# Optimization experiments

Hardware: AMD Instinct MI355X
Metric: run time of the kernel (lower is better)

## Reference

```python
import jax, jax.numpy as jnp
from jax import lax
import numpy as np

B, T, D_IN, H, D_L1_IN = 128, 2048, 5, 128, 256


def _gru_layer(x, w_ih, w_hh, b_ih, b_hh, reverse):
    # x: [B,T,D]; w_ih: [3H,D]; w_hh: [3H,H]. PyTorch gate order: r, z, n.
    gx = jnp.einsum('btd,gd->btg', x, w_ih) + b_ih  # [B,T,3H] input projections, batched
    if reverse:
        gx = gx[:, ::-1]
    gx_t = jnp.swapaxes(gx, 0, 1)  # [T,B,3H]
    h0 = jnp.zeros((x.shape[0], H), x.dtype)

    def step(h, gxt):
        gh = h @ w_hh.T + b_hh  # [B,3H]
        r = jax.nn.sigmoid(gxt[:, :H] + gh[:, :H])
        z = jax.nn.sigmoid(gxt[:, H:2 * H] + gh[:, H:2 * H])
        n = jnp.tanh(gxt[:, 2 * H:] + r * gh[:, 2 * H:])
        h_new = (1.0 - z) * n + z * h
        return h_new, h_new

    _, ys = lax.scan(step, h0, gx_t)  # ys: [T,B,H]
    ys = jnp.swapaxes(ys, 0, 1)  # [B,T,H]
    if reverse:
        ys = ys[:, ::-1]
    return ys


def setup_inputs() -> dict:
    key = jax.random.key(0)
    ks = jax.random.split(key, 16)
    s0 = 1.0 / np.sqrt(H)

    def w(k, shape):
        return jax.random.uniform(k, shape, jnp.float32, -s0, s0)

    inp = {'seq': jax.random.normal(ks[0], (B, T, D_IN), jnp.float32)}
    # layer 0 forward / backward (input dim 5)
    inp['w_ih_l0f'] = w(ks[1], (3 * H, D_IN)); inp['w_hh_l0f'] = w(ks[2], (3 * H, H))
    inp['b_ih_l0f'] = w(ks[3], (3 * H,));      inp['b_hh_l0f'] = w(ks[4], (3 * H,))
    inp['w_ih_l0b'] = w(ks[5], (3 * H, D_IN)); inp['w_hh_l0b'] = w(ks[6], (3 * H, H))
    inp['b_ih_l0b'] = w(ks[7], (3 * H,));      inp['b_hh_l0b'] = w(ks[8], (3 * H,))
    # layer 1 forward / backward (input dim 256 = 2*H)
    inp['w_ih_l1f'] = w(ks[9], (3 * H, D_L1_IN));  inp['w_hh_l1f'] = w(ks[10], (3 * H, H))
    inp['b_ih_l1f'] = w(ks[11], (3 * H,));         inp['b_hh_l1f'] = w(ks[12], (3 * H,))
    inp['w_ih_l1b'] = w(ks[13], (3 * H, D_L1_IN)); inp['w_hh_l1b'] = w(ks[14], (3 * H, H))
    inp['b_ih_l1b'] = w(ks[15], (3 * H,));         inp['b_hh_l1b'] = w(ks[15], (3 * H,)) * 0.9
    # linear head
    kf = jax.random.split(ks[0], 2)
    inp['fc_w'] = w(kf[0], (1, 2 * H))
    inp['fc_b'] = w(kf[1], (1,))
    return inp


def reference(seq, w_ih_l0f, w_hh_l0f, b_ih_l0f, b_hh_l0f,
              w_ih_l0b, w_hh_l0b, b_ih_l0b, b_hh_l0b,
              w_ih_l1f, w_hh_l1f, b_ih_l1f, b_hh_l1f,
              w_ih_l1b, w_hh_l1b, b_ih_l1b, b_hh_l1b,
              fc_w, fc_b):
    # layer 0: bidirectional, concat directions
    y0f = _gru_layer(seq, w_ih_l0f, w_hh_l0f, b_ih_l0f, b_hh_l0f, reverse=False)
    y0b = _gru_layer(seq, w_ih_l0b, w_hh_l0b, b_ih_l0b, b_hh_l0b, reverse=True)
    y0 = jnp.concatenate([y0f, y0b], axis=-1)  # [B,T,256]
    # layer 1
    y1f = _gru_layer(y0, w_ih_l1f, w_hh_l1f, b_ih_l1f, b_hh_l1f, reverse=False)
    y1b = _gru_layer(y0, w_ih_l1b, w_hh_l1b, b_ih_l1b, b_hh_l1b, reverse=True)
    y1 = jnp.concatenate([y1f, y1b], axis=-1)  # [B,T,256]
    # head on last timestep
    return y1[:, -1, :] @ fc_w.T + fc_b  # [B,1]
```

## Files before the change

### kernel.cpp

```cpp
#include <hip/hip_runtime.h>
#include <hip/hip_fp16.h>
#include <cstdint>

#define B_   128
#define T_   2048
#define DIN  5
#define H_   128
#define G3   384
#define D1   256
#define CH   128
#define NCH  (T_ / CH)
#define LOG2CH 7
#define NTILE (B_ * CH / 128 * 6)
#define NGB   248

typedef _Float16 half8 __attribute__((ext_vector_type(8)));
typedef float f32x4 __attribute__((ext_vector_type(4)));

__device__ __forceinline__ float sigmoid_f(float x) {
    return __builtin_amdgcn_rcpf(1.0f + __expf(-x));
}
__device__ __forceinline__ float tanh_f(float x) {
    return 1.0f - 2.0f * __builtin_amdgcn_rcpf(__expf(2.0f * x) + 1.0f);
}
__device__ __forceinline__ unsigned long long pack4h(const float* h) {
    union { __half2 h2[2]; unsigned long long u; } pk;
    pk.h2[0] = __floats2half2_rn(h[0], h[1]);
    pk.h2[1] = __floats2half2_rn(h[2], h[3]);
    return pk.u;
}
__device__ __forceinline__ f32x4 h4_to_f(unsigned long long u) {
    union { unsigned long long u; __half2 h2[2]; } p; p.u = u;
    const float2 a = __half22float2(p.h2[0]);
    const float2 b = __half22float2(p.h2[1]);
    f32x4 r; r[0] = a.x; r[1] = a.y; r[2] = b.x; r[3] = b.y; return r;
}
__device__ __forceinline__ void fast_barrier() {
    asm volatile("s_waitcnt lgkmcnt(0)\n\ts_barrier" ::: "memory");
}

__global__ __launch_bounds__(512, 2) void scan0_mfma4(
    const float* __restrict__ seq,
    const float* __restrict__ wihf, const float* __restrict__ whhf,
    const float* __restrict__ bihf, const float* __restrict__ bhhf,
    const float* __restrict__ wihb, const float* __restrict__ whhb,
    const float* __restrict__ bihb, const float* __restrict__ bhhb,
    __half* __restrict__ y0)
{
    const int tid = threadIdx.x;
    const int w  = tid >> 6;
    const int l  = tid & 63;
    const int lo = l & 15;
    const int g  = l >> 4;
    const int dir = blockIdx.x >> 3;
    const int bg  = blockIdx.x & 7;

    const float* w_ih = dir ? wihb : wihf;
    const float* w_hh = dir ? whhb : whhf;
    const float* b_ih = dir ? bihb : bihf;
    const float* b_hh = dir ? bhhb : bhhf;

    __shared__ __align__(16) char smem[2 * 16 * 512];

    half8 a_r[5], a_z[5], a_n[5], a_x;
    {
        const int grow = w * 16 + lo;
#pragma unroll
        for (int c = 0; c < 5; ++c) {
            half8 vr, vz, vn;
#pragma unroll
            for (int j = 0; j < 8; ++j) {
                const int k = c * 32 + g * 8 + j;
                float fr, fz, fn;
                if (k < 128) {
                    fr = w_hh[grow * H_ + k];
                    fz = w_hh[(128 + grow) * H_ + k];
                    fn = w_hh[(256 + grow) * H_ + k];
                } else if (k < 133) {
                    fr = w_ih[grow * DIN + (k - 128)];
                    fz = w_ih[(128 + grow) * DIN + (k - 128)];
                    fn = 0.f;
                } else if (k == 133) {
                    fr = b_ih[grow] + b_hh[grow];
                    fz = b_ih[128 + grow] + b_hh[128 + grow];
                    fn = b_hh[256 + grow];
                } else { fr = 0.f; fz = 0.f; fn = 0.f; }
                vr[j] = (_Float16)fr; vz[j] = (_Float16)fz; vn[j] = (_Float16)fn;
            }
            a_r[c] = vr; a_z[c] = vz; a_n[c] = vn;
        }
        half8 vx;
#pragma unroll
        for (int j = 0; j < 8; ++j) {
            const int k = 128 + g * 8 + j;
            float f = 0.f;
            if (k < 133)       f = w_ih[(256 + grow) * DIN + (k - 128)];
            else if (k == 133) f = b_ih[256 + grow];
            vx[j] = (_Float16)f;
        }
        a_x = vx;
    }

#pragma unroll
    for (int q = 0; q < 2; ++q) {
        f32x4 z = {0.f, 0.f, 0.f, 0.f};
        *reinterpret_cast<f32x4*>(smem + tid * 32 + q * 16) = z;
    }
    __syncthreads();
    if (tid < 32) {
        const int row = tid & 15, bu = tid >> 4;
        *(_Float16*)(smem + bu * 8192 + row * 512 + (266 ^ ((row & 7) << 4))) =
            (_Float16)1.0f;
    }
    const bool stager = tid < 80;
    const int sb = tid / 5, sd = tid % 5;
    const size_t seqbase = (size_t)(bg * 16 + sb) * T_ * DIN + sd;
    float x_t1 = 0.f;
    if (stager) {
        const int tt0 = dir ? (T_ - 1) : 0;
        const float x0 = seq[seqbase + (size_t)tt0 * DIN];
        *(_Float16*)(smem + sb * 512 + ((256 + 2 * sd) ^ ((sb & 7) << 4))) =
            (_Float16)x0;
        const int tt1 = dir ? (T_ - 2) : 1;
        x_t1 = seq[seqbase + (size_t)tt1 * DIN];
    }
    __syncthreads();

    float h_old[4];
#pragma unroll
    for (int q = 0; q < 4; ++q) h_old[q] = 0.f;

    for (int t = 0; t < T_; ++t) {
        char* cur = smem + (t & 1) * 8192;
        char* nxt = smem + ((t + 1) & 1) * 8192;

        if (stager)
            *(_Float16*)(nxt + sb * 512 + ((256 + 2 * sd) ^ ((sb & 7) << 4))) =
                (_Float16)x_t1;

        half8 bf[5];
#pragma unroll
        for (int c = 0; c < 5; ++c)
            bf[c] = *reinterpret_cast<const half8*>(
                cur + lo * 512 + ((c * 64 + g * 16) ^ ((lo & 7) << 4)));

        float x_t2 = 0.f;
        if (stager) {
            const int t2 = (t + 2 < T_) ? t + 2 : T_ - 1;
            const int tt2 = dir ? (T_ - 1 - t2) : t2;
            x_t2 = seq[seqbase + (size_t)tt2 * DIN];
        }

        f32x4 zr = {0.f, 0.f, 0.f, 0.f};
        f32x4 accr = zr, accz = zr, accn = zr, accx;
#pragma unroll
        for (int c = 0; c < 5; ++c) {
            accr = __builtin_amdgcn_mfma_f32_16x16x32_f16(a_r[c], bf[c], accr, 0, 0, 0);
            accz = __builtin_amdgcn_mfma_f32_16x16x32_f16(a_z[c], bf[c], accz, 0, 0, 0);
            accn = __builtin_amdgcn_mfma_f32_16x16x32_f16(a_n[c], bf[c], accn, 0, 0, 0);
        }
        accx = __builtin_amdgcn_mfma_f32_16x16x32_f16(a_x, bf[4], zr, 0, 0, 0);

        const int tt = dir ? (T_ - 1 - t) : t;
        {
            float hn[4];
#pragma unroll
            for (int q = 0; q < 4; ++q) {
                const float r = sigmoid_f(accr[q]);
                const float z = sigmoid_f(accz[q]);
                const float n = tanh_f(accx[q] + r * accn[q]);
                hn[q] = n + z * (h_old[q] - n);
                h_old[q] = hn[q];
            }
            const int j0 = w * 16 + g * 4;
            const unsigned long long pu = pack4h(hn);
            *reinterpret_cast<unsigned long long*>(
                &y0[((size_t)(bg * 16 + lo) * T_ + tt) * D1 + dir * H_ + j0]) = pu;
            *reinterpret_cast<unsigned long long*>(
                nxt + lo * 512 + ((2 * j0) ^ ((lo & 7) << 4))) = pu;
        }
        x_t1 = x_t2;
        fast_barrier();
    }
}

__device__ __forceinline__ void scan1_role(
    char* smem,
    const __half* __restrict__ gxc,
    const float* __restrict__ whh, const float* __restrict__ bhh,
    float* __restrict__ h1, int c)
{
    __builtin_amdgcn_s_setprio(1);

    const int tid = threadIdx.x;
    const int w = tid >> 6, l = tid & 63;
    const int lo = l & 15, g = l >> 4;
    const int grp = blockIdx.x;

    half8 a_r[2][4], a_z[2][4], a_n[2][4];
    float br[2][4], bz[2][4], bn[2][4];
#pragma unroll
    for (int i = 0; i < 2; ++i) {
        const int grow = (2 * w + i) * 16 + lo;
#pragma unroll
        for (int cc = 0; cc < 4; ++cc) {
            half8 vr, vz, vn;
#pragma unroll
            for (int j = 0; j < 8; ++j) {
                const int k = cc * 32 + g * 8 + j;
                vr[j] = (_Float16)whh[grow * H_ + k];
                vz[j] = (_Float16)whh[(128 + grow) * H_ + k];
                vn[j] = (_Float16)whh[(256 + grow) * H_ + k];
            }
            a_r[i][cc] = vr; a_z[i][cc] = vz; a_n[i][cc] = vn;
        }
#pragma unroll
        for (int q = 0; q < 4; ++q) {
            const int gq = (2 * w + i) * 16 + g * 4 + q;
            br[i][q] = bhh[gq];
            bz[i][q] = bhh[128 + gq];
            bn[i][q] = bhh[256 + gq];
        }
    }

#pragma unroll
    for (int q = 0; q < 2; ++q) {
        f32x4 z = {0.f, 0.f, 0.f, 0.f};
        *reinterpret_cast<f32x4*>(smem + tid * 32 + q * 16) = z;
    }
    __syncthreads();

    float h_old[2][4];
    if (c == 0) {
#pragma unroll
        for (int i = 0; i < 2; ++i)
#pragma unroll
            for (int q = 0; q < 4; ++q) h_old[i][q] = 0.f;
    } else {
#pragma unroll
        for (int i = 0; i < 2; ++i) {
            const int j0 = (2 * w + i) * 16 + g * 4;
            const f32x4 hv = *reinterpret_cast<const f32x4*>(
                &h1[(grp * 16 + lo) * H_ + j0]);
            float hn[4];
#pragma unroll
            for (int q = 0; q < 4; ++q) { h_old[i][q] = hv[q]; hn[q] = hv[q]; }
            *reinterpret_cast<unsigned long long*>(
                smem + lo * 256 + ((2 * j0) ^ ((lo & 7) << 4))) = pack4h(hn);
        }
    }
    __syncthreads();

    const __half* gxl = gxc + (size_t)(grp * 16 + lo) * CH * G3;
    unsigned long long gxc_cur[6], gxc_nxt[6];
#pragma unroll
    for (int i = 0; i < 2; ++i) {
        const int gr0 = (2 * w + i) * 16 + g * 4;
        gxc_cur[i]     = *reinterpret_cast<const unsigned long long*>(gxl + gr0);
        gxc_cur[2 + i] = *reinterpret_cast<const unsigned long long*>(gxl + 128 + gr0);
        gxc_cur[4 + i] = *reinterpret_cast<const unsigned long long*>(gxl + 256 + gr0);
    }

    for (int t = 0; t < CH; ++t) {
        char* curb = smem + (t & 1) * 4096;
        char* nxtb = smem + ((t + 1) & 1) * 4096;

        half8 bf[4];
#pragma unroll
        for (int cc = 0; cc < 4; ++cc)
            bf[cc] = *reinterpret_cast<const half8*>(
                curb + lo * 256 + ((cc * 64 + g * 16) ^ ((lo & 7) << 4)));

        const int tn = (t + 1 < CH) ? t + 1 : t;
        const __half* p = gxl + (size_t)tn * G3;
#pragma unroll
        for (int i = 0; i < 2; ++i) {
            const int gr0 = (2 * w + i) * 16 + g * 4;
            gxc_nxt[i]     = *reinterpret_cast<const unsigned long long*>(p + gr0);
            gxc_nxt[2 + i] = *reinterpret_cast<const unsigned long long*>(p + 128 + gr0);
            gxc_nxt[4 + i] = *reinterpret_cast<const unsigned long long*>(p + 256 + gr0);
        }

        f32x4 accr[2], accz[2], accn[2];
#pragma unroll
        for (int i = 0; i < 2; ++i) {
            f32x4 zr = {0.f, 0.f, 0.f, 0.f};
            accr[i] = zr; accz[i] = zr; accn[i] = zr;
#pragma unroll
            for (int cc = 0; cc < 4; ++cc) {
                accr[i] = __builtin_amdgcn_mfma_f32_16x16x32_f16(a_r[i][cc], bf[cc], accr[i], 0, 0, 0);
                accz[i] = __builtin_amdgcn_mfma_f32_16x16x32_f16(a_z[i][cc], bf[cc], accz[i], 0, 0, 0);
                accn[i] = __builtin_amdgcn_mfma_f32_16x16x32_f16(a_n[i][cc], bf[cc], accn[i], 0, 0, 0);
            }
        }

#pragma unroll
        for (int i = 0; i < 2; ++i) {
            const f32x4 gr = h4_to_f(gxc_cur[i]);
            const f32x4 gz = h4_to_f(gxc_cur[2 + i]);
            const f32x4 gn = h4_to_f(gxc_cur[4 + i]);
            float hn[4];
#pragma unroll
            for (int q = 0; q < 4; ++q) {
                const float r = sigmoid_f(accr[i][q] + br[i][q] + gr[q]);
                const float z = sigmoid_f(accz[i][q] + bz[i][q] + gz[q]);
                const float n = tanh_f(gn[q] + r * (accn[i][q] + bn[i][q]));
                hn[q] = n + z * (h_old[i][q] - n);
                h_old[i][q] = hn[q];
            }
            const int j0 = (2 * w + i) * 16 + g * 4;
            *reinterpret_cast<unsigned long long*>(
                nxtb + lo * 256 + ((2 * j0) ^ ((lo & 7) << 4))) = pack4h(hn);
        }
#pragma unroll
        for (int i = 0; i < 6; ++i) gxc_cur[i] = gxc_nxt[i];
        fast_barrier();
    }

#pragma unroll
    for (int i = 0; i < 2; ++i) {
        const int j0 = (2 * w + i) * 16 + g * 4;
        f32x4 hv;
#pragma unroll
        for (int q = 0; q < 4; ++q) hv[q] = h_old[i][q];
        *reinterpret_cast<f32x4*>(&h1[(grp * 16 + lo) * H_ + j0]) = hv;
    }
    __builtin_amdgcn_s_setprio(0);
}

__device__ __forceinline__ void gemm_role(
    char* smem, int rb,
    const __half* __restrict__ A, const float* __restrict__ W,
    const float* __restrict__ bias, __half* __restrict__ C, int c0)
{
    _Float16 (*As)[32] = reinterpret_cast<_Float16(*)[32]>(smem);
    _Float16 (*Bs)[32] = reinterpret_cast<_Float16(*)[32]>(smem + 8192);
    const int tid = threadIdx.x;
    const int wave = tid >> 6, l = tid & 63;
    const int wm = wave >> 1, wn = wave & 1;
    const int lo = l & 15, g = l >> 4;
    const int m0 = (rb & 127) * 128, n0 = (rb >> 7) * 64;

    f32x4 acc[4][2];
#pragma unroll
    for (int mt = 0; mt < 4; ++mt)
#pragma unroll
        for (int nt = 0; nt < 2; ++nt) {
            f32x4 z = {0.f, 0.f, 0.f, 0.f};
            acc[mt][nt] = z;
        }

    for (int kc = 0; kc < 256; kc += 32) {
#pragma unroll
        for (int r2 = 0; r2 < 2; ++r2) {
            const int idx = tid + r2 * 256;
            const int row = idx >> 2, seg = idx & 3;
            const int m = m0 + row, bb = m >> LOG2CH, tlq = m & (CH - 1);
            const __half* src = A + ((size_t)bb * T_ + c0 + tlq) * D1 + kc + seg * 8;
            *reinterpret_cast<uint4*>(&As[row][seg * 8]) =
                *reinterpret_cast<const uint4*>(src);
        }
        {
            const int row = tid >> 2, seg = tid & 3;
            const float* srcw = W + (size_t)(n0 + row) * D1 + kc + seg * 8;
            const float4 u0 = *reinterpret_cast<const float4*>(srcw);
            const float4 u1 = *reinterpret_cast<const float4*>(srcw + 4);
            half8 hv;
            hv[0] = (_Float16)u0.x; hv[1] = (_Float16)u0.y;
            hv[2] = (_Float16)u0.z; hv[3] = (_Float16)u0.w;
            hv[4] = (_Float16)u1.x; hv[5] = (_Float16)u1.y;
            hv[6] = (_Float16)u1.z; hv[7] = (_Float16)u1.w;
            *reinterpret_cast<half8*>(&Bs[row][seg * 8]) = hv;
        }
        __syncthreads();
        half8 af[4], bfr[2];
#pragma unroll
        for (int mt = 0; mt < 4; ++mt)
            af[mt] = *reinterpret_cast<half8*>(&As[wm * 64 + mt * 16 + lo][g * 8]);
#pragma unroll
        for (int nt = 0; nt < 2; ++nt)
            bfr[nt] = *reinterpret_cast<half8*>(&Bs[wn * 32 + nt * 16 + lo][g * 8]);
#pragma unroll
        for (int mt = 0; mt < 4; ++mt)
#pragma unroll
            for (int nt = 0; nt < 2; ++nt)
                acc[mt][nt] = __builtin_amdgcn_mfma_f32_16x16x32_f16(
                    af[mt], bfr[nt], acc[mt][nt], 0, 0, 0);
        __syncthreads();
    }
#pragma unroll
    for (int nt = 0; nt < 2; ++nt) {
        const int n = n0 + wn * 32 + nt * 16 + lo;
        const float bv = bias[n];
#pragma unroll
        for (int mt = 0; mt < 4; ++mt) {
            const int mrow = m0 + wm * 64 + mt * 16 + g * 4;
#pragma unroll
            for (int q = 0; q < 4; ++q)
                C[(size_t)(mrow + q) * G3 + n] = __float2half(acc[mt][nt][q] + bv);
        }
    }
}

__global__ __launch_bounds__(256, 1) void fused_l1(
    const __half* __restrict__ y0,
    const float* __restrict__ W1f, const float* __restrict__ b1f,
    __half* __restrict__ gbufA, __half* __restrict__ gbufB,
    const float* __restrict__ whh, const float* __restrict__ bhh,
    float* __restrict__ h1, int ci_scan, int ci_gemm)
{
    __shared__ __align__(16) char smem[12288];
    if (blockIdx.x < 8) {
        if (ci_scan >= 0) {
            const __half* gxc = (ci_scan & 1) ? gbufB : gbufA;
            scan1_role(smem, gxc, whh, bhh, h1, ci_scan);
        }
    } else {
        if (ci_gemm < NCH) {
            __half* gxc = (ci_gemm & 1) ? gbufB : gbufA;
            for (int rb = (int)blockIdx.x - 8; rb < NTILE; rb += NGB)
                gemm_role(smem, rb, y0, W1f, b1f, gxc, ci_gemm * CH);
        }
    }
}

__global__ __launch_bounds__(384, 1) void back1_fc(
    const __half* __restrict__ y0, const float* __restrict__ h1,
    const float* __restrict__ w_ih_1b, const float* __restrict__ b_ih_1b,
    const float* __restrict__ b_hh_1b,
    const float* __restrict__ fc_w, const float* __restrict__ fc_b,
    float* __restrict__ out)
{
    const int g = threadIdx.x;
    const int b = blockIdx.x;
    __shared__ float ylast[D1];
    __shared__ float pre_rz[2 * H_];
    __shared__ float gxn[H_], ghn[H_];
    __shared__ float hb[H_];
    __shared__ float red[H_];

    if (g < D1) ylast[g] = __half2float(y0[((size_t)b * T_ + (T_ - 1)) * D1 + g]);
    __syncthreads();

    float accb = b_ih_1b[g];
    const float* wrow = w_ih_1b + (size_t)g * D1;
#pragma unroll 8
    for (int k = 0; k < D1; k += 4) {
        const float4 v = *reinterpret_cast<const float4*>(&ylast[k]);
        const float4 wv = *reinterpret_cast<const float4*>(&wrow[k]);
        accb += v.x * wv.x + v.y * wv.y + v.z * wv.z + v.w * wv.w;
    }
    const float bh2 = b_hh_1b[g];
    if (g < 2 * H_) pre_rz[g] = accb + bh2;
    else            { gxn[g - 2 * H_] = accb; ghn[g - 2 * H_] = bh2; }
    __syncthreads();
    if (g < H_) {
        const float r = sigmoid_f(pre_rz[g]);
        const float z = sigmoid_f(pre_rz[g + H_]);
        const float n = tanh_f(gxn[g] + r * ghn[g]);
        hb[g] = (1.0f - z) * n;
    }
    __syncthreads();
    if (g < H_) red[g] = h1[b * H_ + g] * fc_w[g] + hb[g] * fc_w[H_ + g];
    __syncthreads();
    if (g == 0) {
        float s = fc_b[0];
#pragma unroll 8
        for (int k = 0; k < H_; ++k) s += red[k];
        out[b] = s;
    }
}

extern "C" void kernel_launch(void* const* d_in, const int* in_sizes, int n_in,
                              void* d_out, int out_size, void* d_ws, size_t ws_size,
                              hipStream_t stream)
{
    const float* seq      = (const float*)d_in[0];
    const float* w_ih_l0f = (const float*)d_in[1];
    const float* w_hh_l0f = (const float*)d_in[2];
    const float* b_ih_l0f = (const float*)d_in[3];
    const float* b_hh_l0f = (const float*)d_in[4];
    const float* w_ih_l0b = (const float*)d_in[5];
    const float* w_hh_l0b = (const float*)d_in[6];
    const float* b_ih_l0b = (const float*)d_in[7];
    const float* b_hh_l0b = (const float*)d_in[8];
    const float* w_ih_l1f = (const float*)d_in[9];
    const float* w_hh_l1f = (const float*)d_in[10];
    const float* b_ih_l1f = (const float*)d_in[11];
    const float* b_hh_l1f = (const float*)d_in[12];
    const float* w_ih_l1b = (const float*)d_in[13];
    const float* b_ih_l1b = (const float*)d_in[15];
    const float* b_hh_l1b = (const float*)d_in[16];
    const float* fc_w     = (const float*)d_in[17];
    const float* fc_b     = (const float*)d_in[18];
    float* out = (float*)d_out;

    const size_t y0_bytes = (size_t)B_ * T_ * D1 * sizeof(__half);
    const size_t gx_bytes = (size_t)B_ * CH * G3 * sizeof(__half);
    __half* y0h   = (__half*)d_ws;
    __half* gbufA = (__half*)((char*)d_ws + y0_bytes);
    __half* gbufB = (__half*)((char*)d_ws + y0_bytes + gx_bytes);
    float*  h1    = (float*)((char*)d_ws + y0_bytes + 2 * gx_bytes);

    hipLaunchKernelGGL(scan0_mfma4, dim3(16), dim3(512), 0, stream,
        seq, w_ih_l0f, w_hh_l0f, b_ih_l0f, b_hh_l0f,
             w_ih_l0b, w_hh_l0b, b_ih_l0b, b_hh_l0b, y0h);

    for (int i = 0; i <= NCH; ++i) {
        hipLaunchKernelGGL(fused_l1, dim3(8 + NGB), dim3(256), 0, stream,
            y0h, w_ih_l1f, b_ih_l1f, gbufA, gbufB,
            w_hh_l1f, b_hh_l1f, h1, i - 1, i);
    }

    hipLaunchKernelGGL(back1_fc, dim3(B_), dim3(384), 0, stream,
        y0h, h1, w_ih_l1b, b_ih_l1b, b_hh_l1b, fc_w, fc_b, out);
}
```

Measured before the change: 3.443 ms.

## Replace per-chunk layer-1 launches with one persistent kernel using flag sync

The 17 per-chunk launches of the fused layer-1 kernel become a single persistent kernel. Scan blocks and GEMM blocks now coordinate through global atomic counters: scan blocks spin until a chunk's GEMM is done, and GEMM blocks wait until the scan has consumed the buffer from two chunks earlier. The scan keeps its hidden state in registers across chunks instead of round-tripping through global memory. This removes kernel-launch and tail overhead and lets the GEMM run ahead, but it relies on all 256 blocks being co-resident and adds spin-wait and fence costs.

```diff
diff --git a/kernel.cpp b/kernel.cpp
--- a/kernel.cpp
+++ b/kernel.cpp
@@ -45,7 +45,7 @@
     const float* __restrict__ bihf, const float* __restrict__ bhhf,
     const float* __restrict__ wihb, const float* __restrict__ whhb,
     const float* __restrict__ bihb, const float* __restrict__ bhhb,
-    __half* __restrict__ y0)
+    __half* __restrict__ y0, int* __restrict__ flags)
 {
     const int tid = threadIdx.x;
     const int w  = tid >> 6;
@@ -54,6 +54,8 @@
     const int g  = l >> 4;
     const int dir = blockIdx.x >> 3;
     const int bg  = blockIdx.x & 7;
+
+    if (blockIdx.x == 0 && tid < 2 * NCH) flags[tid] = 0;
 
     const float* w_ih = dir ? wihb : wihf;
     const float* w_hh = dir ? whhb : whhf;
@@ -184,150 +186,6 @@
     }
 }
 
-__device__ __forceinline__ void scan1_role(
-    char* smem,
-    const __half* __restrict__ gxc,
-    const float* __restrict__ whh, const float* __restrict__ bhh,
-    float* __restrict__ h1, int c)
-{
-    __builtin_amdgcn_s_setprio(1);
-
-    const int tid = threadIdx.x;
-    const int w = tid >> 6, l = tid & 63;
-    const int lo = l & 15, g = l >> 4;
-    const int grp = blockIdx.x;
-
-    half8 a_r[2][4], a_z[2][4], a_n[2][4];
-    float br[2][4], bz[2][4], bn[2][4];
-#pragma unroll
-    for (int i = 0; i < 2; ++i) {
-        const int grow = (2 * w + i) * 16 + lo;
-#pragma unroll
-        for (int cc = 0; cc < 4; ++cc) {
-            half8 vr, vz, vn;
-#pragma unroll
-            for (int j = 0; j < 8; ++j) {
-                const int k = cc * 32 + g * 8 + j;
-                vr[j] = (_Float16)whh[grow * H_ + k];
-                vz[j] = (_Float16)whh[(128 + grow) * H_ + k];
-                vn[j] = (_Float16)whh[(256 + grow) * H_ + k];
-            }
-            a_r[i][cc] = vr; a_z[i][cc] = vz; a_n[i][cc] = vn;
-        }
-#pragma unroll
-        for (int q = 0; q < 4; ++q) {
-            const int gq = (2 * w + i) * 16 + g * 4 + q;
-            br[i][q] = bhh[gq];
-            bz[i][q] = bhh[128 + gq];
-            bn[i][q] = bhh[256 + gq];
-        }
-    }
-
-#pragma unroll
-    for (int q = 0; q < 2; ++q) {
-        f32x4 z = {0.f, 0.f, 0.f, 0.f};
-        *reinterpret_cast<f32x4*>(smem + tid * 32 + q * 16) = z;
-    }
-    __syncthreads();
-
-    float h_old[2][4];
-    if (c == 0) {
-#pragma unroll
-        for (int i = 0; i < 2; ++i)
-#pragma unroll
-            for (int q = 0; q < 4; ++q) h_old[i][q] = 0.f;
-    } else {
-#pragma unroll
-        for (int i = 0; i < 2; ++i) {
-            const int j0 = (2 * w + i) * 16 + g * 4;
-            const f32x4 hv = *reinterpret_cast<const f32x4*>(
-                &h1[(grp * 16 + lo) * H_ + j0]);
-            float hn[4];
-#pragma unroll
-            for (int q = 0; q < 4; ++q) { h_old[i][q] = hv[q]; hn[q] = hv[q]; }
-            *reinterpret_cast<unsigned long long*>(
-                smem + lo * 256 + ((2 * j0) ^ ((lo & 7) << 4))) = pack4h(hn);
-        }
-    }
-    __syncthreads();
-
-    const __half* gxl = gxc + (size_t)(grp * 16 + lo) * CH * G3;
-    unsigned long long gxc_cur[6], gxc_nxt[6];
-#pragma unroll
-    for (int i = 0; i < 2; ++i) {
-        const int gr0 = (2 * w + i) * 16 + g * 4;
-        gxc_cur[i]     = *reinterpret_cast<const unsigned long long*>(gxl + gr0);
-        gxc_cur[2 + i] = *reinterpret_cast<const unsigned long long*>(gxl + 128 + gr0);
-        gxc_cur[4 + i] = *reinterpret_cast<const unsigned long long*>(gxl + 256 + gr0);
-    }
-
-    for (int t = 0; t < CH; ++t) {
-        char* curb = smem + (t & 1) * 4096;
-        char* nxtb = smem + ((t + 1) & 1) * 4096;
-
-        half8 bf[4];
-#pragma unroll
-        for (int cc = 0; cc < 4; ++cc)
-            bf[cc] = *reinterpret_cast<const half8*>(
-                curb + lo * 256 + ((cc * 64 + g * 16) ^ ((lo & 7) << 4)));
-
-        const int tn = (t + 1 < CH) ? t + 1 : t;
-        const __half* p = gxl + (size_t)tn * G3;
-#pragma unroll
-        for (int i = 0; i < 2; ++i) {
-            const int gr0 = (2 * w + i) * 16 + g * 4;
-            gxc_nxt[i]     = *reinterpret_cast<const unsigned long long*>(p + gr0);
-            gxc_nxt[2 + i] = *reinterpret_cast<const unsigned long long*>(p + 128 + gr0);
-            gxc_nxt[4 + i] = *reinterpret_cast<const unsigned long long*>(p + 256 + gr0);
-        }
-
-        f32x4 accr[2], accz[2], accn[2];
-#pragma unroll
-        for (int i = 0; i < 2; ++i) {
-            f32x4 zr = {0.f, 0.f, 0.f, 0.f};
-            accr[i] = zr; accz[i] = zr; accn[i] = zr;
-#pragma unroll
-            for (int cc = 0; cc < 4; ++cc) {
-                accr[i] = __builtin_amdgcn_mfma_f32_16x16x32_f16(a_r[i][cc], bf[cc], accr[i], 0, 0, 0);
-                accz[i] = __builtin_amdgcn_mfma_f32_16x16x32_f16(a_z[i][cc], bf[cc], accz[i], 0, 0, 0);
-                accn[i] = __builtin_amdgcn_mfma_f32_16x16x32_f16(a_n[i][cc], bf[cc], accn[i], 0, 0, 0);
-            }
-        }
-
-#pragma unroll
-        for (int i = 0; i < 2; ++i) {
-            const f32x4 gr = h4_to_f(gxc_cur[i]);
-            const f32x4 gz = h4_to_f(gxc_cur[2 + i]);
-            const f32x4 gn = h4_to_f(gxc_cur[4 + i]);
-            float hn[4];
-#pragma unroll
-            for (int q = 0; q < 4; ++q) {
-                const float r = sigmoid_f(accr[i][q] + br[i][q] + gr[q]);
-                const float z = sigmoid_f(accz[i][q] + bz[i][q] + gz[q]);
-                const float n = tanh_f(gn[q] + r * (accn[i][q] + bn[i][q]));
-                hn[q] = n + z * (h_old[i][q] - n);
-                h_old[i][q] = hn[q];
-            }
-            const int j0 = (2 * w + i) * 16 + g * 4;
-            *reinterpret_cast<unsigned long long*>(
-                nxtb + lo * 256 + ((2 * j0) ^ ((lo & 7) << 4))) = pack4h(hn);
-        }
-#pragma unroll
-        for (int i = 0; i < 6; ++i) gxc_cur[i] = gxc_nxt[i];
-        fast_barrier();
-    }
-
-#pragma unroll
-    for (int i = 0; i < 2; ++i) {
-        const int j0 = (2 * w + i) * 16 + g * 4;
-        f32x4 hv;
-#pragma unroll
-        for (int q = 0; q < 4; ++q) hv[q] = h_old[i][q];
-        *reinterpret_cast<f32x4*>(&h1[(grp * 16 + lo) * H_ + j0]) = hv;
-    }
-    __builtin_amdgcn_s_setprio(0);
-}
-
 __device__ __forceinline__ void gemm_role(
     char* smem, int rb,
     const __half* __restrict__ A, const float* __restrict__ W,
@@ -402,24 +260,171 @@
     }
 }
 
-__global__ __launch_bounds__(256, 1) void fused_l1(
+__global__ __launch_bounds__(256, 1) void fused_l1_persist(
     const __half* __restrict__ y0,
     const float* __restrict__ W1f, const float* __restrict__ b1f,
     __half* __restrict__ gbufA, __half* __restrict__ gbufB,
     const float* __restrict__ whh, const float* __restrict__ bhh,
-    float* __restrict__ h1, int ci_scan, int ci_gemm)
+    float* __restrict__ h1, int* __restrict__ gemm_done,
+    int* __restrict__ scan_done)
 {
     __shared__ __align__(16) char smem[12288];
+    const int tid = threadIdx.x;
+
     if (blockIdx.x < 8) {
-        if (ci_scan >= 0) {
-            const __half* gxc = (ci_scan & 1) ? gbufB : gbufA;
-            scan1_role(smem, gxc, whh, bhh, h1, ci_scan);
-        }
+        __builtin_amdgcn_s_setprio(1);
+        const int w = tid >> 6, l = tid & 63;
+        const int lo = l & 15, g = l >> 4;
+        const int grp = blockIdx.x;
+
+        half8 a_r[2][4], a_z[2][4], a_n[2][4];
+        float br[2][4], bz[2][4], bn[2][4];
+#pragma unroll
+        for (int i = 0; i < 2; ++i) {
+            const int grow = (2 * w + i) * 16 + lo;
+#pragma unroll
+            for (int cc = 0; cc < 4; ++cc) {
+                half8 vr, vz, vn;
+#pragma unroll
+                for (int j = 0; j < 8; ++j) {
+                    const int k = cc * 32 + g * 8 + j;
+                    vr[j] = (_Float16)whh[grow * H_ + k];
+                    vz[j] = (_Float16)whh[(128 + grow) * H_ + k];
+                    vn[j] = (_Float16)whh[(256 + grow) * H_ + k];
+                }
+                a_r[i][cc] = vr; a_z[i][cc] = vz; a_n[i][cc] = vn;
+            }
+#pragma unroll
+            for (int q = 0; q < 4; ++q) {
+                const int gq = (2 * w + i) * 16 + g * 4 + q;
+                br[i][q] = bhh[gq];
+                bz[i][q] = bhh[128 + gq];
+                bn[i][q] = bhh[256 + gq];
+            }
+        }
+
+#pragma unroll
+        for (int q = 0; q < 2; ++q) {
+            f32x4 z = {0.f, 0.f, 0.f, 0.f};
+            *reinterpret_cast<f32x4*>(smem + tid * 32 + q * 16) = z;
+        }
+        __syncthreads();
+
+        float h_old[2][4];
+#pragma unroll
+        for (int i = 0; i < 2; ++i)
+#pragma unroll
+            for (int q = 0; q < 4; ++q) h_old[i][q] = 0.f;
+
+        for (int c = 0; c < NCH; ++c) {
+            if (tid == 0) {
+                while (__hip_atomic_load(&gemm_done[c], __ATOMIC_ACQUIRE,
+                                         __HIP_MEMORY_SCOPE_AGENT) < NGB)
+                    __builtin_amdgcn_s_sleep(2);
+            }
+            __syncthreads();
+            __threadfence();
+
+            const __half* gxc = (c & 1) ? gbufB : gbufA;
+            const __half* gxl = gxc + (size_t)(grp * 16 + lo) * CH * G3;
+            unsigned long long gxc_cur[6], gxc_nxt[6];
+#pragma unroll
+            for (int i = 0; i < 2; ++i) {
+                const int gr0 = (2 * w + i) * 16 + g * 4;
+                gxc_cur[i]     = *reinterpret_cast<const unsigned long long*>(gxl + gr0);
+                gxc_cur[2 + i] = *reinterpret_cast<const unsigned long long*>(gxl + 128 + gr0);
+                gxc_cur[4 + i] = *reinterpret_cast<const unsigned long long*>(gxl + 256 + gr0);
+            }
+
+            for (int t = 0; t < CH; ++t) {
+                char* curb = smem + (t & 1) * 4096;
+                char* nxtb = smem + ((t + 1) & 1) * 4096;
+
+                half8 bf[4];
+#pragma unroll
+                for (int cc = 0; cc < 4; ++cc)
+                    bf[cc] = *reinterpret_cast<const half8*>(
+                        curb + lo * 256 + ((cc * 64 + g * 16) ^ ((lo & 7) << 4)));
+
+                const int tn = (t + 1 < CH) ? t + 1 : t;
+                const __half* p = gxl + (size_t)tn * G3;
+#pragma unroll
+                for (int i = 0; i < 2; ++i) {
+                    const int gr0 = (2 * w + i) * 16 + g * 4;
+                    gxc_nxt[i]     = *reinterpret_cast<const unsigned long long*>(p + gr0);
+                    gxc_nxt[2 + i] = *reinterpret_cast<const unsigned long long*>(p + 128 + gr0);
+                    gxc_nxt[4 + i] = *reinterpret_cast<const unsigned long long*>(p + 256 + gr0);
+                }
+
+                f32x4 accr[2], accz[2], accn[2];
+#pragma unroll
+                for (int i = 0; i < 2; ++i) {
+                    f32x4 zr = {0.f, 0.f, 0.f, 0.f};
+                    accr[i] = zr; accz[i] = zr; accn[i] = zr;
+#pragma unroll
+                    for (int cc = 0; cc < 4; ++cc) {
+                        accr[i] = __builtin_amdgcn_mfma_f32_16x16x32_f16(a_r[i][cc], bf[cc], accr[i], 0, 0, 0);
+                        accz[i] = __builtin_amdgcn_mfma_f32_16x16x32_f16(a_z[i][cc], bf[cc], accz[i], 0, 0, 0);
+                        accn[i] = __builtin_amdgcn_mfma_f32_16x16x32_f16(a_n[i][cc], bf[cc], accn[i], 0, 0, 0);
+                    }
+                }
+
+#pragma unroll
+                for (int i = 0; i < 2; ++i) {
+                    const f32x4 gr = h4_to_f(gxc_cur[i]);
+                    const f32x4 gz = h4_to_f(gxc_cur[2 + i]);
+                    const f32x4 gn = h4_to_f(gxc_cur[4 + i]);
+                    float hn[4];
+#pragma unroll
+                    for (int q = 0; q < 4; ++q) {
+                        const float r = sigmoid_f(accr[i][q] + br[i][q] + gr[q]);
+                        const float z = sigmoid_f(accz[i][q] + bz[i][q] + gz[q]);
+                        const float n = tanh_f(gn[q] + r * (accn[i][q] + bn[i][q]));
+                        hn[q] = n + z * (h_old[i][q] - n);
+                        h_old[i][q] = hn[q];
+                    }
+                    const int j0 = (2 * w + i) * 16 + g * 4;
+                    *reinterpret_cast<unsigned long long*>(
+                        nxtb + lo * 256 + ((2 * j0) ^ ((lo & 7) << 4))) = pack4h(hn);
+                }
+#pragma unroll
+                for (int i = 0; i < 6; ++i) gxc_cur[i] = gxc_nxt[i];
+                fast_barrier();
+            }
+
+            __syncthreads();
+            if (tid == 0)
+                __hip_atomic_fetch_add(&scan_done[c], 1, __ATOMIC_RELEASE,
+                                       __HIP_MEMORY_SCOPE_AGENT);
+        }
+
+#pragma unroll
+        for (int i = 0; i < 2; ++i) {
+            const int j0 = (2 * w + i) * 16 + g * 4;
+            f32x4 hv;
+#pragma unroll
+            for (int q = 0; q < 4; ++q) hv[q] = h_old[i][q];
+            *reinterpret_cast<f32x4*>(&h1[(grp * 16 + lo) * H_ + j0]) = hv;
+        }
+        __builtin_amdgcn_s_setprio(0);
     } else {
-        if (ci_gemm < NCH) {
-            __half* gxc = (ci_gemm & 1) ? gbufB : gbufA;
+        for (int c = 0; c < NCH; ++c) {
+            if (c >= 2) {
+                if (tid == 0) {
+                    while (__hip_atomic_load(&scan_done[c - 2], __ATOMIC_ACQUIRE,
+                                             __HIP_MEMORY_SCOPE_AGENT) < 8)
+                        __builtin_amdgcn_s_sleep(2);
+                }
+                __syncthreads();
+            }
+            __half* gxc = (c & 1) ? gbufB : gbufA;
             for (int rb = (int)blockIdx.x - 8; rb < NTILE; rb += NGB)
-                gemm_role(smem, rb, y0, W1f, b1f, gxc, ci_gemm * CH);
+                gemm_role(smem, rb, y0, W1f, b1f, gxc, c * CH);
+            __threadfence();
+            __syncthreads();
+            if (tid == 0)
+                __hip_atomic_fetch_add(&gemm_done[c], 1, __ATOMIC_RELEASE,
+                                       __HIP_MEMORY_SCOPE_AGENT);
         }
     }
 }
@@ -501,16 +506,17 @@
     __half* gbufA = (__half*)((char*)d_ws + y0_bytes);
     __half* gbufB = (__half*)((char*)d_ws + y0_bytes + gx_bytes);
     float*  h1    = (float*)((char*)d_ws + y0_bytes + 2 * gx_bytes);
+    int*    flags = (int*)(h1 + B_ * H_);
+    int* gemm_done = flags;
+    int* scan_done = flags + NCH;
 
     hipLaunchKernelGGL(scan0_mfma4, dim3(16), dim3(512), 0, stream,
         seq, w_ih_l0f, w_hh_l0f, b_ih_l0f, b_hh_l0f,
-             w_ih_l0b, w_hh_l0b, b_ih_l0b, b_hh_l0b, y0h);
-
-    for (int i = 0; i <= NCH; ++i) {
-        hipLaunchKernelGGL(fused_l1, dim3(8 + NGB), dim3(256), 0, stream,
-            y0h, w_ih_l1f, b_ih_l1f, gbufA, gbufB,
-            w_hh_l1f, b_hh_l1f, h1, i - 1, i);
-    }
+             w_ih_l0b, w_hh_l0b, b_ih_l0b, b_hh_l0b, y0h, flags);
+
+    hipLaunchKernelGGL(fused_l1_persist, dim3(8 + NGB), dim3(256), 0, stream,
+        y0h, w_ih_l1f, b_ih_l1f, gbufA, gbufB,
+        w_hh_l1f, b_hh_l1f, h1, gemm_done, scan_done);
 
     hipLaunchKernelGGL(back1_fc, dim3(B_), dim3(384), 0, stream,
         y0h, h1, w_ih_l1b, b_ih_l1b, b_hh_l1b, fc_w, fc_b, out);
```

Measured after the change: 5.876 ms. +70.6%, slower.
